# Performance work log

Hardware: AMD Instinct MI355X
Metric: run time of the kernel (lower is better)

## Reference

```python
import jax, jax.numpy as jnp
import numpy as np

HIDDEN_DIM = 2048
NUM_HEADS = 16
HEAD_DIM = HIDDEN_DIM // NUM_HEADS


def setup_inputs() -> dict:
    key = jax.random.key(0)
    ks = jax.random.split(key, 5)
    B, S, D = 2, 2048, HIDDEN_DIM
    scale = 1.0 / np.sqrt(D)
    return {
        "x": jax.random.normal(ks[0], (B, S, D), dtype=jnp.float32),
        "w_q": jax.random.normal(ks[1], (D, D), dtype=jnp.float32) * scale,
        "w_k": jax.random.normal(ks[2], (D, D), dtype=jnp.float32) * scale,
        "w_v": jax.random.normal(ks[3], (D, D), dtype=jnp.float32) * scale,
        "w_o": jax.random.normal(ks[4], (D, D), dtype=jnp.float32) * scale,
        "causal": 1,
    }


def _attention(q, k, v, causal):
    # q,k,v: (B, S, D) -> split heads -> (B, H, S, d)
    B, S, D = q.shape
    q = q.reshape(B, S, NUM_HEADS, HEAD_DIM).transpose(0, 2, 1, 3)
    k = k.reshape(B, S, NUM_HEADS, HEAD_DIM).transpose(0, 2, 1, 3)
    v = v.reshape(B, S, NUM_HEADS, HEAD_DIM).transpose(0, 2, 1, 3)
    scale = 1.0 / np.sqrt(HEAD_DIM)
    # scores: (B, H, S, S)
    s = jnp.einsum("bhqd,bhkd->bhqk", q, k) * scale
    if causal:
        qpos = jnp.arange(S)[:, None]
        kpos = jnp.arange(S)[None, :]
        s = jnp.where(kpos > qpos, -jnp.inf, s)
    # stable softmax; rows that are fully -inf cannot occur with causal mask
    p = jax.nn.softmax(s, axis=-1)
    o = jnp.einsum("bhqk,bhkd->bhqd", p, v)
    return o.transpose(0, 2, 1, 3).reshape(B, S, D)


def reference(x, w_q, w_k, w_v, w_o, causal):
    q = x @ w_q.T
    k = x @ w_k.T
    v = x @ w_v.T
    o = _attention(q, k, v, bool(causal))
    return o @ w_o.T
```

## Files before the change

kernel.cpp:

```cpp
#include <hip/hip_runtime.h>


typedef __attribute__((ext_vector_type(8))) short short8;
typedef __attribute__((ext_vector_type(4))) short bfs4;
typedef __attribute__((ext_vector_type(4))) float floatx4;

__device__ __forceinline__ void gl_lds16(const void* g, void* l) {
  __builtin_amdgcn_global_load_lds((const __attribute__((address_space(1))) void*)g,
                                   (__attribute__((address_space(3))) void*)l, 16, 0, 0);
}

__device__ __forceinline__ short f2bf(float f) {
  union { float f; unsigned u; } a; a.f = f;
  unsigned r = a.u + 0x7FFFu + ((a.u >> 16) & 1u);
  return (short)(r >> 16);
}

__global__ __launch_bounds__(256) void cvt_bf16(
    const float* __restrict__ s0, const float* __restrict__ s1,
    const float* __restrict__ s2, const float* __restrict__ s3,
    const float* __restrict__ s4,
    short* __restrict__ d0, short* __restrict__ d1, short* __restrict__ d2,
    short* __restrict__ d3, short* __restrict__ d4,
    int n0, int nw) {
  const int z = blockIdx.z;
  const float* s = (z == 0) ? s0 : (z == 1) ? s1 : (z == 2) ? s2 : (z == 3) ? s3 : s4;
  short* d      = (z == 0) ? d0 : (z == 1) ? d1 : (z == 2) ? d2 : (z == 3) ? d3 : d4;
  const int n   = (z == 0) ? n0 : nw;
  const int stride = gridDim.x * blockDim.x * 4;
  for (int i = (blockIdx.x * blockDim.x + threadIdx.x) * 4; i < n; i += stride) {
    float4 v = *(const float4*)(s + i);
    bfs4 o;
    o[0] = f2bf(v.x); o[1] = f2bf(v.y); o[2] = f2bf(v.z); o[3] = f2bf(v.w);
    *(bfs4*)(d + i) = o;
  }
}

__global__ __launch_bounds__(256, 2) void gemm_bt(
    const short* __restrict__ A,
    const short* __restrict__ B0, const short* __restrict__ B1, const short* __restrict__ B2,
    short* __restrict__ C0, short* __restrict__ C1, short* __restrict__ C2,
    int M, int N, int K) {
  const short* Bm = (blockIdx.z == 0) ? B0 : ((blockIdx.z == 1) ? B1 : B2);
  short* C = (blockIdx.z == 0) ? C0 : ((blockIdx.z == 1) ? C1 : C2);

  __shared__ short As[128 * 64];
  __shared__ short Bs[128 * 64];

  const int tid = threadIdx.x;
  const int w = tid >> 6, l = tid & 63;
  const int lane15 = l & 15, quad = l >> 4;
  const int wr = w >> 1, wc = w & 1;
  const int row0 = blockIdx.y * 128;
  const int col0 = blockIdx.x * 128;

  floatx4 acc[4][4] = {};
  const int srow = l >> 3;
  const int sg = l & 7;

  for (int k0 = 0; k0 < K; k0 += 64) {
#pragma unroll
    for (int j = 0; j < 4; ++j) {
      int chunk = j * 4 + w;
      int row = chunk * 8 + srow;
      int g = sg ^ (row & 7);
      gl_lds16(A  + (size_t)(row0 + row) * K + k0 + g * 8, &As[chunk * 512]);
      gl_lds16(Bm + (size_t)(col0 + row) * K + k0 + g * 8, &Bs[chunk * 512]);
    }
    __syncthreads();
#pragma unroll
    for (int ks = 0; ks < 2; ++ks) {
      short8 af[4], bf[4];
#pragma unroll
      for (int i = 0; i < 4; ++i) {
        int rowA = wr * 64 + i * 16 + lane15;
        af[i] = *(const short8*)&As[rowA * 64 + (((ks * 4 + quad) ^ (rowA & 7)) << 3)];
        int rowB = wc * 64 + i * 16 + lane15;
        bf[i] = *(const short8*)&Bs[rowB * 64 + (((ks * 4 + quad) ^ (rowB & 7)) << 3)];
      }
#pragma unroll
      for (int i = 0; i < 4; ++i)
#pragma unroll
        for (int jj = 0; jj < 4; ++jj)
          acc[i][jj] = __builtin_amdgcn_mfma_f32_16x16x32_bf16(af[i], bf[jj], acc[i][jj], 0, 0, 0);
    }
    __syncthreads();
  }

#pragma unroll
  for (int i = 0; i < 4; ++i)
#pragma unroll
    for (int jj = 0; jj < 4; ++jj)
#pragma unroll
      for (int r = 0; r < 4; ++r) {
        int row = row0 + wr * 64 + i * 16 + quad * 4 + r;
        int col = col0 + wc * 64 + jj * 16 + lane15;
        C[(size_t)row * N + col] = f2bf(acc[i][jj][r]);
      }
}

__global__ __launch_bounds__(256, 2) void gemm_bt_f32out(
    const short* __restrict__ A, const short* __restrict__ Bm,
    float* __restrict__ C, int M, int N, int K) {
  __shared__ short As[128 * 64];
  __shared__ short Bs[128 * 64];

  const int tid = threadIdx.x;
  const int w = tid >> 6, l = tid & 63;
  const int lane15 = l & 15, quad = l >> 4;
  const int wr = w >> 1, wc = w & 1;
  const int row0 = blockIdx.y * 128;
  const int col0 = blockIdx.x * 128;

  floatx4 acc[4][4] = {};
  const int srow = l >> 3;
  const int sg = l & 7;

  for (int k0 = 0; k0 < K; k0 += 64) {
#pragma unroll
    for (int j = 0; j < 4; ++j) {
      int chunk = j * 4 + w;
      int row = chunk * 8 + srow;
      int g = sg ^ (row & 7);
      gl_lds16(A  + (size_t)(row0 + row) * K + k0 + g * 8, &As[chunk * 512]);
      gl_lds16(Bm + (size_t)(col0 + row) * K + k0 + g * 8, &Bs[chunk * 512]);
    }
    __syncthreads();
#pragma unroll
    for (int ks = 0; ks < 2; ++ks) {
      short8 af[4], bf[4];
#pragma unroll
      for (int i = 0; i < 4; ++i) {
        int rowA = wr * 64 + i * 16 + lane15;
        af[i] = *(const short8*)&As[rowA * 64 + (((ks * 4 + quad) ^ (rowA & 7)) << 3)];
        int rowB = wc * 64 + i * 16 + lane15;
        bf[i] = *(const short8*)&Bs[rowB * 64 + (((ks * 4 + quad) ^ (rowB & 7)) << 3)];
      }
#pragma unroll
      for (int i = 0; i < 4; ++i)
#pragma unroll
        for (int jj = 0; jj < 4; ++jj)
          acc[i][jj] = __builtin_amdgcn_mfma_f32_16x16x32_bf16(af[i], bf[jj], acc[i][jj], 0, 0, 0);
    }
    __syncthreads();
  }

#pragma unroll
  for (int i = 0; i < 4; ++i)
#pragma unroll
    for (int jj = 0; jj < 4; ++jj)
#pragma unroll
      for (int r = 0; r < 4; ++r) {
        int row = row0 + wr * 64 + i * 16 + quad * 4 + r;
        int col = col0 + wc * 64 + jj * 16 + lane15;
        C[(size_t)row * N + col] = acc[i][jj][r];
      }
}

__global__ __launch_bounds__(256, 2) void attn_fused(
    const short* __restrict__ Qg, const short* __restrict__ Kg,
    const short* __restrict__ Vg, short* __restrict__ Og,
    const int* __restrict__ causal_p) {
  constexpr int S = 2048, D = 2048, HDim = 128, KT = 32;
  constexpr int PS = 40;
  __shared__ short smem[10880];
  short* Qs = smem;
  short* Ks = smem;
  short* Vt = smem + 4096;
  short* Ps = smem + 8192;
  float* aLds = (float*)(smem + 10752);

  const int tid = threadIdx.x;
  const int w = tid >> 6, l = tid & 63;
  const int lane15 = l & 15, quad = l >> 4;
  const int bh = blockIdx.y, b = bh >> 4, h = bh & 15;
  const size_t rbase = (size_t)b * S;
  const int c0 = h * HDim;
  const int causal = *causal_p;
  short* Pw = Ps + w * (16 * PS);
  constexpr float SCL = 0.08838834764831845f * 1.4426950408889634f;

  const int vs = tid & 31;
  const int vdg = tid >> 5;

#pragma unroll 1
  for (int ph = 0; ph < 2; ++ph) {
    const int jt = ph ? (31 - blockIdx.x) : blockIdx.x;
    const int q0 = jt * 64;
    const int wrow0 = q0 + w * 16;

#pragma unroll
    for (int j = 0; j < 4; ++j) {
      int chunk = j * 4 + w;
      int row = chunk * 4 + quad;
      int g = lane15 ^ (row & 7);
      gl_lds16(Qg + (rbase + q0 + row) * D + c0 + g * 8, &Qs[chunk * 512]);
    }
    __syncthreads();
    short8 qf[4];
#pragma unroll
    for (int ks = 0; ks < 4; ++ks) {
      int row = w * 16 + lane15;
      qf[ks] = *(const short8*)&Qs[row * HDim + (((ks * 4 + quad) ^ (row & 7)) << 3)];
    }
    __syncthreads();

    floatx4 ot[8] = {};
    float psum[4] = {0.f, 0.f, 0.f, 0.f};
    const int ktiles = causal ? (q0 / KT + 2) : (S / KT);

    for (int kt = 0; kt < ktiles; ++kt) {
      const int k0 = kt * KT;
#pragma unroll
      for (int j = 0; j < 2; ++j) {
        int chunk = j * 4 + w;
        int row = chunk * 4 + quad;
        int g = lane15 ^ (row & 7);
        gl_lds16(Kg + (rbase + k0 + row) * D + c0 + g * 8, &Ks[chunk * 512]);
      }
      {
        const short* vp = Vg + (rbase + k0 + vs) * D + c0 + vdg * 16;
        short8 v0 = *(const short8*)vp;
        short8 v1 = *(const short8*)(vp + 8);
        int sg8 = vs >> 3, so = vs & 7;
#pragma unroll
        for (int e = 0; e < 8; ++e) {
          int d0 = vdg * 16 + e, d1 = vdg * 16 + 8 + e;
          Vt[d0 * 32 + ((sg8 ^ (d0 & 3)) << 3) + so] = v0[e];
          Vt[d1 * 32 + ((sg8 ^ (d1 & 3)) << 3) + so] = v1[e];
        }
      }
      __syncthreads();

      if (!causal || k0 <= wrow0 + 15) {
        floatx4 sacc[2] = {};
#pragma unroll
        for (int ks = 0; ks < 4; ++ks) {
          short8 kf0, kf1;
          {
            int row = lane15;
            kf0 = *(const short8*)&Ks[row * HDim + (((ks * 4 + quad) ^ (row & 7)) << 3)];
            row = 16 + lane15;
            kf1 = *(const short8*)&Ks[row * HDim + (((ks * 4 + quad) ^ (row & 7)) << 3)];
          }
          sacc[0] = __builtin_amdgcn_mfma_f32_16x16x32_bf16(qf[ks], kf0, sacc[0], 0, 0, 0);
          sacc[1] = __builtin_amdgcn_mfma_f32_16x16x32_bf16(qf[ks], kf1, sacc[1], 0, 0, 0);
        }
#pragma unroll
        for (int r = 0; r < 4; ++r) {
          int prow = quad * 4 + r;
          int qrow = wrow0 + prow;
          float s0 = fminf(sacc[0][r] * SCL, 115.0f);
          float s1 = fminf(sacc[1][r] * SCL, 115.0f);
          float p0 = exp2f(s0);
          float p1 = exp2f(s1);
          if (causal) {
            if (k0 + lane15 > qrow)      p0 = 0.f;
            if (k0 + 16 + lane15 > qrow) p1 = 0.f;
          }
          psum[r] += p0 + p1;
          Pw[prow * PS + lane15]      = f2bf(p0);
          Pw[prow * PS + 16 + lane15] = f2bf(p1);
        }
        short8 pf = *(const short8*)&Pw[lane15 * PS + quad * 8];
#pragma unroll
        for (int cd = 0; cd < 8; ++cd) {
          int d = cd * 16 + lane15;
          short8 vf = *(const short8*)&Vt[d * 32 + ((quad ^ (d & 3)) << 3)];
          ot[cd] = __builtin_amdgcn_mfma_f32_16x16x32_bf16(vf, pf, ot[cd], 0, 0, 0);
        }
      }
      __syncthreads();
    }

#pragma unroll
    for (int r = 0; r < 4; ++r) {
      float s = psum[r];
      s += __shfl_xor(s, 1, 64);
      s += __shfl_xor(s, 2, 64);
      s += __shfl_xor(s, 4, 64);
      s += __shfl_xor(s, 8, 64);
      if (lane15 == 0) aLds[w * 16 + quad * 4 + r] = 1.0f / s;
    }
    float invq = aLds[w * 16 + lane15];

#pragma unroll
    for (int cd = 0; cd < 8; ++cd)
#pragma unroll
      for (int r = 0; r < 4; ++r) {
        int row = w * 16 + lane15;
        int col = cd * 16 + quad * 4 + r;
        Qs[row * HDim + (((col >> 3) ^ (row & 7)) << 3) + (col & 7)] =
            f2bf(ot[cd][r] * invq);
      }
    __syncthreads();
#pragma unroll
    for (int i = 0; i < 4; ++i) {
      int c = i * 256 + tid;
      int row = c >> 4, g = c & 15;
      *(short8*)(Og + (rbase + q0 + row) * D + c0 + g * 8) =
          *(const short8*)&Qs[row * HDim + ((g ^ (row & 7)) << 3)];
    }
    __syncthreads();
  }
}

extern "C" void kernel_launch(void* const* d_in, const int* in_sizes, int n_in,
                              void* d_out, int out_size, void* d_ws, size_t ws_size,
                              hipStream_t stream) {
  const float* x  = (const float*)d_in[0];
  const float* wq = (const float*)d_in[1];
  const float* wk = (const float*)d_in[2];
  const float* wv = (const float*)d_in[3];
  const float* wo = (const float*)d_in[4];
  const int* causal = (const int*)d_in[5];
  float* out = (float*)d_out;

  const int M = 4096, N = 2048, K = 2048;
  const int NX = M * K;
  const int NW = N * K;

  char* ws = (char*)d_ws;
  short* xb  = (short*)(ws);
  short* wqb = (short*)(ws + 16u * 1024 * 1024);
  short* wkb = (short*)(ws + 24u * 1024 * 1024);
  short* wvb = (short*)(ws + 32u * 1024 * 1024);
  short* wob = (short*)(ws + 40u * 1024 * 1024);
  short* q   = (short*)(ws + 48u * 1024 * 1024);
  short* k   = (short*)(ws + 64u * 1024 * 1024);
  short* v   = (short*)(ws + 80u * 1024 * 1024);
  short* o   = (short*)(ws + 96u * 1024 * 1024);

  dim3 blk(256);
  cvt_bf16<<<dim3(2048, 1, 5), blk, 0, stream>>>(x, wq, wk, wv, wo,
                                                 xb, wqb, wkb, wvb, wob, NX, NW);
  gemm_bt<<<dim3(N / 128, M / 128, 3), blk, 0, stream>>>(xb, wqb, wkb, wvb,
                                                         q, k, v, M, N, K);
  attn_fused<<<dim3(16, 32), blk, 0, stream>>>(q, k, v, o, causal);
  gemm_bt_f32out<<<dim3(N / 128, M / 128, 1), blk, 0, stream>>>(o, wob, out, M, N, K);
}
```

Before: 384.4 us.

## Double-buffer K/V tiles in attention and split q-tile pairs into separate blocks

The attention kernel now prefetches the next K tile (async global-to-LDS) and the next V tile (into registers) while computing on the current one, using ping-pong LDS buffers, so each iteration needs one barrier instead of two. The two-phase balanced loop over q-tile pairs is removed and the grid doubles to one q-tile per block, with launch bounds raised to 4 blocks per CU. The V transpose store is reworked to write packed 32-bit pairs with a new swizzle. The cost is more LDS per block and register pressure under the tighter launch bound, plus the causal load imbalance that the paired scheduling used to hide.

```diff
diff --git a/kernel.cpp b/kernel.cpp
--- a/kernel.cpp
+++ b/kernel.cpp
@@ -157,18 +157,20 @@
       }
 }
 
-__global__ __launch_bounds__(256, 2) void attn_fused(
+__global__ __launch_bounds__(256, 4) void attn_fused(
     const short* __restrict__ Qg, const short* __restrict__ Kg,
     const short* __restrict__ Vg, short* __restrict__ Og,
     const int* __restrict__ causal_p) {
   constexpr int S = 2048, D = 2048, HDim = 128, KT = 32;
   constexpr int PS = 40;
-  __shared__ short smem[10880];
-  short* Qs = smem;
-  short* Ks = smem;
-  short* Vt = smem + 4096;
-  short* Ps = smem + 8192;
-  float* aLds = (float*)(smem + 10752);
+  __shared__ short smem[19072];
+  short* Qs  = smem;
+  short* Ks0 = smem;
+  short* Ks1 = smem + 4096;
+  short* Vt0 = smem + 8192;
+  short* Vt1 = smem + 12288;
+  short* Ps  = smem + 16384;
+  float* aLds = (float*)(smem + 18944);
 
   const int tid = threadIdx.x;
   const int w = tid >> 6, l = tid & 63;
@@ -180,128 +182,157 @@
   short* Pw = Ps + w * (16 * PS);
   constexpr float SCL = 0.08838834764831845f * 1.4426950408889634f;
 
-  const int vs = tid & 31;
-  const int vdg = tid >> 5;
-
-#pragma unroll 1
-  for (int ph = 0; ph < 2; ++ph) {
-    const int jt = ph ? (31 - blockIdx.x) : blockIdx.x;
-    const int q0 = jt * 64;
-    const int wrow0 = q0 + w * 16;
-
-#pragma unroll
-    for (int j = 0; j < 4; ++j) {
-      int chunk = j * 4 + w;
-      int row = chunk * 4 + quad;
-      int g = lane15 ^ (row & 7);
-      gl_lds16(Qg + (rbase + q0 + row) * D + c0 + g * 8, &Qs[chunk * 512]);
-    }
-    __syncthreads();
-    short8 qf[4];
-#pragma unroll
-    for (int ks = 0; ks < 4; ++ks) {
-      int row = w * 16 + lane15;
-      qf[ks] = *(const short8*)&Qs[row * HDim + (((ks * 4 + quad) ^ (row & 7)) << 3)];
-    }
-    __syncthreads();
-
-    floatx4 ot[8] = {};
-    float psum[4] = {0.f, 0.f, 0.f, 0.f};
-    const int ktiles = causal ? (q0 / KT + 2) : (S / KT);
-
-    for (int kt = 0; kt < ktiles; ++kt) {
-      const int k0 = kt * KT;
+  const int vdg = tid & 15;
+  const int vs0 = (tid >> 4) * 2;
+  const int vsg = vs0 >> 3;
+  const int vso = vs0 & 7;
+
+  const int jt = 31 - blockIdx.x;
+  const int q0 = jt * 64;
+  const int wrow0 = q0 + w * 16;
+
+#pragma unroll
+  for (int j = 0; j < 4; ++j) {
+    int chunk = j * 4 + w;
+    int row = chunk * 4 + quad;
+    int g = lane15 ^ (row & 7);
+    gl_lds16(Qg + (rbase + q0 + row) * D + c0 + g * 8, &Qs[chunk * 512]);
+  }
+  __syncthreads();
+  short8 qf[4];
+#pragma unroll
+  for (int ks = 0; ks < 4; ++ks) {
+    int row = w * 16 + lane15;
+    qf[ks] = *(const short8*)&Qs[row * HDim + (((ks * 4 + quad) ^ (row & 7)) << 3)];
+  }
+  __syncthreads();
+
+  floatx4 ot[8] = {};
+  float psum[4] = {0.f, 0.f, 0.f, 0.f};
+  const int ktiles = causal ? (q0 / KT + 2) : (S / KT);
+
+#pragma unroll
+  for (int j = 0; j < 2; ++j) {
+    int chunk = j * 4 + w;
+    int row = chunk * 4 + quad;
+    int g = lane15 ^ (row & 7);
+    gl_lds16(Kg + (rbase + row) * D + c0 + g * 8, &Ks0[chunk * 512]);
+  }
+  {
+    const short* vp = Vg + (rbase + vs0) * D + c0 + vdg * 8;
+    short8 v0 = *(const short8*)vp;
+    short8 v1 = *(const short8*)(vp + D);
+#pragma unroll
+    for (int e = 0; e < 8; ++e) {
+      int d = vdg * 8 + e;
+      int g = (vsg ^ (d ^ (d >> 2))) & 3;
+      *(int*)&Vt0[d * 32 + (g << 3) + vso] =
+          (int)(unsigned short)v0[e] | ((int)(unsigned short)v1[e] << 16);
+    }
+  }
+  __syncthreads();
+
+  short* Kc = Ks0; short* Kn = Ks1;
+  short* Vc = Vt0; short* Vn = Vt1;
+
+  for (int kt = 0; kt < ktiles; ++kt) {
+    const int k0 = kt * KT;
+    const bool pf = (kt + 1 < ktiles);
+    short8 pv0, pv1;
+    if (pf) {
 #pragma unroll
       for (int j = 0; j < 2; ++j) {
         int chunk = j * 4 + w;
         int row = chunk * 4 + quad;
         int g = lane15 ^ (row & 7);
-        gl_lds16(Kg + (rbase + k0 + row) * D + c0 + g * 8, &Ks[chunk * 512]);
-      }
-      {
-        const short* vp = Vg + (rbase + k0 + vs) * D + c0 + vdg * 16;
-        short8 v0 = *(const short8*)vp;
-        short8 v1 = *(const short8*)(vp + 8);
-        int sg8 = vs >> 3, so = vs & 7;
-#pragma unroll
-        for (int e = 0; e < 8; ++e) {
-          int d0 = vdg * 16 + e, d1 = vdg * 16 + 8 + e;
-          Vt[d0 * 32 + ((sg8 ^ (d0 & 3)) << 3) + so] = v0[e];
-          Vt[d1 * 32 + ((sg8 ^ (d1 & 3)) << 3) + so] = v1[e];
+        gl_lds16(Kg + (rbase + k0 + KT + row) * D + c0 + g * 8, &Kn[chunk * 512]);
+      }
+      const short* vp = Vg + (rbase + k0 + KT + vs0) * D + c0 + vdg * 8;
+      pv0 = *(const short8*)vp;
+      pv1 = *(const short8*)(vp + D);
+    }
+
+    if (!causal || k0 <= wrow0 + 15) {
+      floatx4 sacc[2] = {};
+#pragma unroll
+      for (int ks = 0; ks < 4; ++ks) {
+        short8 kf0, kf1;
+        {
+          int row = lane15;
+          kf0 = *(const short8*)&Kc[row * HDim + (((ks * 4 + quad) ^ (row & 7)) << 3)];
+          row = 16 + lane15;
+          kf1 = *(const short8*)&Kc[row * HDim + (((ks * 4 + quad) ^ (row & 7)) << 3)];
         }
-      }
-      __syncthreads();
-
-      if (!causal || k0 <= wrow0 + 15) {
-        floatx4 sacc[2] = {};
-#pragma unroll
-        for (int ks = 0; ks < 4; ++ks) {
-          short8 kf0, kf1;
-          {
-            int row = lane15;
-            kf0 = *(const short8*)&Ks[row * HDim + (((ks * 4 + quad) ^ (row & 7)) << 3)];
-            row = 16 + lane15;
-            kf1 = *(const short8*)&Ks[row * HDim + (((ks * 4 + quad) ^ (row & 7)) << 3)];
-          }
-          sacc[0] = __builtin_amdgcn_mfma_f32_16x16x32_bf16(qf[ks], kf0, sacc[0], 0, 0, 0);
-          sacc[1] = __builtin_amdgcn_mfma_f32_16x16x32_bf16(qf[ks], kf1, sacc[1], 0, 0, 0);
+        sacc[0] = __builtin_amdgcn_mfma_f32_16x16x32_bf16(qf[ks], kf0, sacc[0], 0, 0, 0);
+        sacc[1] = __builtin_amdgcn_mfma_f32_16x16x32_bf16(qf[ks], kf1, sacc[1], 0, 0, 0);
+      }
+#pragma unroll
+      for (int r = 0; r < 4; ++r) {
+        int prow = quad * 4 + r;
+        int qrow = wrow0 + prow;
+        float s0 = fminf(sacc[0][r] * SCL, 115.0f);
+        float s1 = fminf(sacc[1][r] * SCL, 115.0f);
+        float p0 = exp2f(s0);
+        float p1 = exp2f(s1);
+        if (causal) {
+          if (k0 + lane15 > qrow)      p0 = 0.f;
+          if (k0 + 16 + lane15 > qrow) p1 = 0.f;
         }
-#pragma unroll
-        for (int r = 0; r < 4; ++r) {
-          int prow = quad * 4 + r;
-          int qrow = wrow0 + prow;
-          float s0 = fminf(sacc[0][r] * SCL, 115.0f);
-          float s1 = fminf(sacc[1][r] * SCL, 115.0f);
-          float p0 = exp2f(s0);
-          float p1 = exp2f(s1);
-          if (causal) {
-            if (k0 + lane15 > qrow)      p0 = 0.f;
-            if (k0 + 16 + lane15 > qrow) p1 = 0.f;
-          }
-          psum[r] += p0 + p1;
-          Pw[prow * PS + lane15]      = f2bf(p0);
-          Pw[prow * PS + 16 + lane15] = f2bf(p1);
-        }
-        short8 pf = *(const short8*)&Pw[lane15 * PS + quad * 8];
-#pragma unroll
-        for (int cd = 0; cd < 8; ++cd) {
-          int d = cd * 16 + lane15;
-          short8 vf = *(const short8*)&Vt[d * 32 + ((quad ^ (d & 3)) << 3)];
-          ot[cd] = __builtin_amdgcn_mfma_f32_16x16x32_bf16(vf, pf, ot[cd], 0, 0, 0);
-        }
-      }
-      __syncthreads();
-    }
-
+        psum[r] += p0 + p1;
+        Pw[prow * PS + lane15]      = f2bf(p0);
+        Pw[prow * PS + 16 + lane15] = f2bf(p1);
+      }
+      short8 pfr = *(const short8*)&Pw[lane15 * PS + quad * 8];
+#pragma unroll
+      for (int cd = 0; cd < 8; ++cd) {
+        int d = cd * 16 + lane15;
+        int g = (quad ^ (d ^ (d >> 2))) & 3;
+        short8 vf = *(const short8*)&Vc[d * 32 + (g << 3)];
+        ot[cd] = __builtin_amdgcn_mfma_f32_16x16x32_bf16(vf, pfr, ot[cd], 0, 0, 0);
+      }
+    }
+
+    if (pf) {
+#pragma unroll
+      for (int e = 0; e < 8; ++e) {
+        int d = vdg * 8 + e;
+        int g = (vsg ^ (d ^ (d >> 2))) & 3;
+        *(int*)&Vn[d * 32 + (g << 3) + vso] =
+            (int)(unsigned short)pv0[e] | ((int)(unsigned short)pv1[e] << 16);
+      }
+    }
+    __syncthreads();
+    short* t = Kc; Kc = Kn; Kn = t;
+    t = Vc; Vc = Vn; Vn = t;
+  }
+
+#pragma unroll
+  for (int r = 0; r < 4; ++r) {
+    float s = psum[r];
+    s += __shfl_xor(s, 1, 64);
+    s += __shfl_xor(s, 2, 64);
+    s += __shfl_xor(s, 4, 64);
+    s += __shfl_xor(s, 8, 64);
+    if (lane15 == 0) aLds[w * 16 + quad * 4 + r] = 1.0f / s;
+  }
+  float invq = aLds[w * 16 + lane15];
+
+#pragma unroll
+  for (int cd = 0; cd < 8; ++cd)
 #pragma unroll
     for (int r = 0; r < 4; ++r) {
-      float s = psum[r];
-      s += __shfl_xor(s, 1, 64);
-      s += __shfl_xor(s, 2, 64);
-      s += __shfl_xor(s, 4, 64);
-      s += __shfl_xor(s, 8, 64);
-      if (lane15 == 0) aLds[w * 16 + quad * 4 + r] = 1.0f / s;
-    }
-    float invq = aLds[w * 16 + lane15];
-
-#pragma unroll
-    for (int cd = 0; cd < 8; ++cd)
-#pragma unroll
-      for (int r = 0; r < 4; ++r) {
-        int row = w * 16 + lane15;
-        int col = cd * 16 + quad * 4 + r;
-        Qs[row * HDim + (((col >> 3) ^ (row & 7)) << 3) + (col & 7)] =
-            f2bf(ot[cd][r] * invq);
-      }
-    __syncthreads();
-#pragma unroll
-    for (int i = 0; i < 4; ++i) {
-      int c = i * 256 + tid;
-      int row = c >> 4, g = c & 15;
-      *(short8*)(Og + (rbase + q0 + row) * D + c0 + g * 8) =
-          *(const short8*)&Qs[row * HDim + ((g ^ (row & 7)) << 3)];
-    }
-    __syncthreads();
+      int row = w * 16 + lane15;
+      int col = cd * 16 + quad * 4 + r;
+      Qs[row * HDim + (((col >> 3) ^ (row & 7)) << 3) + (col & 7)] =
+          f2bf(ot[cd][r] * invq);
+    }
+  __syncthreads();
+#pragma unroll
+  for (int i = 0; i < 4; ++i) {
+    int c = i * 256 + tid;
+    int row = c >> 4, g = c & 15;
+    *(short8*)(Og + (rbase + q0 + row) * D + c0 + g * 8) =
+        *(const short8*)&Qs[row * HDim + ((g ^ (row & 7)) << 3)];
   }
 }
 
@@ -336,6 +367,6 @@
                                                  xb, wqb, wkb, wvb, wob, NX, NW);
   gemm_bt<<<dim3(N / 128, M / 128, 3), blk, 0, stream>>>(xb, wqb, wkb, wvb,
                                                          q, k, v, M, N, K);
-  attn_fused<<<dim3(16, 32), blk, 0, stream>>>(q, k, v, o, causal);
+  attn_fused<<<dim3(32, 32), blk, 0, stream>>>(q, k, v, o, causal);
   gemm_bt_f32out<<<dim3(N / 128, M / 128, 1), blk, 0, stream>>>(o, wob, out, M, N, K);
 }
```

Result: slower. 447.4 us (+16.4%).

## Split attention KV range across two wave groups with 512-thread blocks

Applied to the files above, without the earlier changes.

The attention block grows to 512 threads. Two groups of four waves each process alternating 32-key tiles of a 64-key step, and their partial outputs and row sums are merged through LDS at the end. The aim is more parallelism per query tile and fewer loop iterations and barriers per key. In exchange it doubles LDS use, adds a cross-group reduction, and the launch bound of 4 may limit registers.

```diff
diff --git a/kernel.cpp b/kernel.cpp
--- a/kernel.cpp
+++ b/kernel.cpp
@@ -157,22 +157,26 @@
       }
 }
 
-__global__ __launch_bounds__(256, 2) void attn_fused(
+__global__ __launch_bounds__(512, 4) void attn_fused(
     const short* __restrict__ Qg, const short* __restrict__ Kg,
     const short* __restrict__ Vg, short* __restrict__ Og,
     const int* __restrict__ causal_p) {
-  constexpr int S = 2048, D = 2048, HDim = 128, KT = 32;
+  constexpr int S = 2048, D = 2048, HDim = 128;
   constexpr int PS = 40;
-  __shared__ short smem[10880];
-  short* Qs = smem;
-  short* Ks = smem;
-  short* Vt = smem + 4096;
-  short* Ps = smem + 8192;
-  float* aLds = (float*)(smem + 10752);
+  __shared__ __align__(16) short smem[21760];
+  short* Qs  = smem;
+  short* Ks0 = smem;
+  short* Ks1 = smem + 4096;
+  short* Vt0 = smem + 8192;
+  short* Vt1 = smem + 12288;
+  short* Ps  = smem + 16384;
+  float* aLds = (float*)(smem + 21504);
+  floatx4* F4 = (floatx4*)smem;
 
   const int tid = threadIdx.x;
   const int w = tid >> 6, l = tid & 63;
   const int lane15 = l & 15, quad = l >> 4;
+  const int w4 = w & 3, grp = w >> 2;
   const int bh = blockIdx.y, b = bh >> 4, h = bh & 15;
   const size_t rbase = (size_t)b * S;
   const int c0 = h * HDim;
@@ -180,58 +184,61 @@
   short* Pw = Ps + w * (16 * PS);
   constexpr float SCL = 0.08838834764831845f * 1.4426950408889634f;
 
-  const int vs = tid & 31;
-  const int vdg = tid >> 5;
+  const int vt8 = tid & 255, vtile = tid >> 8;
+  const int vs = vt8 & 31, vdg = vt8 >> 5;
+  const int sg8 = vs >> 3, so = vs & 7;
+  short* Vtb = vtile ? Vt1 : Vt0;
 
 #pragma unroll 1
   for (int ph = 0; ph < 2; ++ph) {
     const int jt = ph ? (31 - blockIdx.x) : blockIdx.x;
     const int q0 = jt * 64;
-    const int wrow0 = q0 + w * 16;
-
-#pragma unroll
-    for (int j = 0; j < 4; ++j) {
-      int chunk = j * 4 + w;
-      int row = chunk * 4 + quad;
-      int g = lane15 ^ (row & 7);
-      gl_lds16(Qg + (rbase + q0 + row) * D + c0 + g * 8, &Qs[chunk * 512]);
+    const int wrow0 = q0 + w4 * 16;
+
+#pragma unroll
+    for (int j = 0; j < 2; ++j) {
+      int row = j * 32 + w * 4 + quad;
+      int gs = lane15 ^ (row & 7);
+      gl_lds16(Qg + (rbase + q0 + row) * D + c0 + gs * 8, &Qs[(j * 8 + w) * 512]);
     }
     __syncthreads();
     short8 qf[4];
 #pragma unroll
     for (int ks = 0; ks < 4; ++ks) {
-      int row = w * 16 + lane15;
+      int row = w4 * 16 + lane15;
       qf[ks] = *(const short8*)&Qs[row * HDim + (((ks * 4 + quad) ^ (row & 7)) << 3)];
     }
     __syncthreads();
 
     floatx4 ot[8] = {};
     float psum[4] = {0.f, 0.f, 0.f, 0.f};
-    const int ktiles = causal ? (q0 / KT + 2) : (S / KT);
-
-    for (int kt = 0; kt < ktiles; ++kt) {
-      const int k0 = kt * KT;
-#pragma unroll
-      for (int j = 0; j < 2; ++j) {
-        int chunk = j * 4 + w;
-        int row = chunk * 4 + quad;
-        int g = lane15 ^ (row & 7);
-        gl_lds16(Kg + (rbase + k0 + row) * D + c0 + g * 8, &Ks[chunk * 512]);
-      }
+    const int ktiles = causal ? (q0 / 32 + 2) : (S / 32);
+    const int iters = ktiles >> 1;
+
+    for (int it = 0; it < iters; ++it) {
+      const int k0A = it * 64;
       {
-        const short* vp = Vg + (rbase + k0 + vs) * D + c0 + vdg * 16;
+        int row = w * 4 + quad;
+        int gs = lane15 ^ (row & 7);
+        gl_lds16(Kg + (rbase + k0A + row) * D + c0 + gs * 8, &Ks0[w * 512]);
+        gl_lds16(Kg + (rbase + k0A + 32 + row) * D + c0 + gs * 8, &Ks1[w * 512]);
+      }
+      {
+        const short* vp = Vg + (rbase + k0A + vtile * 32 + vs) * D + c0 + vdg * 16;
         short8 v0 = *(const short8*)vp;
         short8 v1 = *(const short8*)(vp + 8);
-        int sg8 = vs >> 3, so = vs & 7;
 #pragma unroll
         for (int e = 0; e < 8; ++e) {
           int d0 = vdg * 16 + e, d1 = vdg * 16 + 8 + e;
-          Vt[d0 * 32 + ((sg8 ^ (d0 & 3)) << 3) + so] = v0[e];
-          Vt[d1 * 32 + ((sg8 ^ (d1 & 3)) << 3) + so] = v1[e];
+          Vtb[d0 * 32 + ((sg8 ^ (d0 & 3)) << 3) + so] = v0[e];
+          Vtb[d1 * 32 + ((sg8 ^ (d1 & 3)) << 3) + so] = v1[e];
         }
       }
       __syncthreads();
 
+      const int k0 = k0A + grp * 32;
+      const short* Kc = grp ? Ks1 : Ks0;
+      const short* Vc = grp ? Vt1 : Vt0;
       if (!causal || k0 <= wrow0 + 15) {
         floatx4 sacc[2] = {};
 #pragma unroll
@@ -239,9 +246,9 @@
           short8 kf0, kf1;
           {
             int row = lane15;
-            kf0 = *(const short8*)&Ks[row * HDim + (((ks * 4 + quad) ^ (row & 7)) << 3)];
+            kf0 = *(const short8*)&Kc[row * HDim + (((ks * 4 + quad) ^ (row & 7)) << 3)];
             row = 16 + lane15;
-            kf1 = *(const short8*)&Ks[row * HDim + (((ks * 4 + quad) ^ (row & 7)) << 3)];
+            kf1 = *(const short8*)&Kc[row * HDim + (((ks * 4 + quad) ^ (row & 7)) << 3)];
           }
           sacc[0] = __builtin_amdgcn_mfma_f32_16x16x32_bf16(qf[ks], kf0, sacc[0], 0, 0, 0);
           sacc[1] = __builtin_amdgcn_mfma_f32_16x16x32_bf16(qf[ks], kf1, sacc[1], 0, 0, 0);
@@ -262,12 +269,12 @@
           Pw[prow * PS + lane15]      = f2bf(p0);
           Pw[prow * PS + 16 + lane15] = f2bf(p1);
         }
-        short8 pf = *(const short8*)&Pw[lane15 * PS + quad * 8];
+        short8 pfr = *(const short8*)&Pw[lane15 * PS + quad * 8];
 #pragma unroll
         for (int cd = 0; cd < 8; ++cd) {
           int d = cd * 16 + lane15;
-          short8 vf = *(const short8*)&Vt[d * 32 + ((quad ^ (d & 3)) << 3)];
-          ot[cd] = __builtin_amdgcn_mfma_f32_16x16x32_bf16(vf, pf, ot[cd], 0, 0, 0);
+          short8 vf = *(const short8*)&Vc[d * 32 + ((quad ^ (d & 3)) << 3)];
+          ot[cd] = __builtin_amdgcn_mfma_f32_16x16x32_bf16(vf, pfr, ot[cd], 0, 0, 0);
         }
       }
       __syncthreads();
@@ -280,23 +287,41 @@
       s += __shfl_xor(s, 2, 64);
       s += __shfl_xor(s, 4, 64);
       s += __shfl_xor(s, 8, 64);
-      if (lane15 == 0) aLds[w * 16 + quad * 4 + r] = 1.0f / s;
-    }
-    float invq = aLds[w * 16 + lane15];
-
-#pragma unroll
-    for (int cd = 0; cd < 8; ++cd)
-#pragma unroll
-      for (int r = 0; r < 4; ++r) {
-        int row = w * 16 + lane15;
-        int col = cd * 16 + quad * 4 + r;
-        Qs[row * HDim + (((col >> 3) ^ (row & 7)) << 3) + (col & 7)] =
-            f2bf(ot[cd][r] * invq);
-      }
-    __syncthreads();
-#pragma unroll
-    for (int i = 0; i < 4; ++i) {
-      int c = i * 256 + tid;
+      if (lane15 == 0) aLds[grp * 64 + w4 * 16 + quad * 4 + r] = s;
+    }
+    if (grp == 1) {
+      int qrow = w4 * 16 + lane15;
+#pragma unroll
+      for (int cd = 0; cd < 8; ++cd)
+        F4[qrow * 32 + ((cd * 4 + quad) ^ ((qrow & 7) << 2))] = ot[cd];
+    }
+    __syncthreads();
+    float invq = 0.f;
+    if (grp == 0) {
+      int qrow = w4 * 16 + lane15;
+      invq = 1.0f / (aLds[qrow] + aLds[64 + qrow]);
+#pragma unroll
+      for (int cd = 0; cd < 8; ++cd) {
+        floatx4 o2 = F4[qrow * 32 + ((cd * 4 + quad) ^ ((qrow & 7) << 2))];
+        ot[cd] += o2;
+      }
+    }
+    __syncthreads();
+    if (grp == 0) {
+      int qrow = w4 * 16 + lane15;
+#pragma unroll
+      for (int cd = 0; cd < 8; ++cd)
+#pragma unroll
+        for (int r = 0; r < 4; ++r) {
+          int col = cd * 16 + quad * 4 + r;
+          Qs[qrow * HDim + (((col >> 3) ^ (qrow & 7)) << 3) + (col & 7)] =
+              f2bf(ot[cd][r] * invq);
+        }
+    }
+    __syncthreads();
+#pragma unroll
+    for (int i = 0; i < 2; ++i) {
+      int c = i * 512 + tid;
       int row = c >> 4, g = c & 15;
       *(short8*)(Og + (rbase + q0 + row) * D + c0 + g * 8) =
           *(const short8*)&Qs[row * HDim + ((g ^ (row & 7)) << 3)];
@@ -336,6 +361,6 @@
                                                  xb, wqb, wkb, wvb, wob, NX, NW);
   gemm_bt<<<dim3(N / 128, M / 128, 3), blk, 0, stream>>>(xb, wqb, wkb, wvb,
                                                          q, k, v, M, N, K);
-  attn_fused<<<dim3(16, 32), blk, 0, stream>>>(q, k, v, o, causal);
+  attn_fused<<<dim3(16, 32), dim3(512), 0, stream>>>(q, k, v, o, causal);
   gemm_bt_f32out<<<dim3(N / 128, M / 128, 1), blk, 0, stream>>>(o, wob, out, M, N, K);
 }
```

New measurement: 396.7 us. 3.2% more time.
